# Optimization experiments

Hardware: AMD Instinct MI355X
Metric: run time of the kernel (lower is better)

The kernel has to match this reference:

```python
import jax, jax.numpy as jnp
import numpy as np

EPS = 1e-5
GROUPS = 8


def setup_inputs() -> dict:
    key = jax.random.key(0)
    ks = jax.random.split(key, 7)
    B, C, L = 16, 512, 4096
    x = jax.random.normal(ks[0], (B, C, L), dtype=jnp.float32)
    gamma = jnp.ones((C,), jnp.float32)
    beta = jnp.zeros((C,), jnp.float32)
    # Conv1d kernel_size=1 weights -> plain matrices
    w1 = jax.random.normal(ks[1], (2 * C, C), jnp.float32) / np.sqrt(C)
    b1 = jax.random.normal(ks[2], (2 * C,), jnp.float32) * 0.01
    w2 = jax.random.normal(ks[3], (C, 2 * C), jnp.float32) / np.sqrt(2 * C)
    b2 = jax.random.normal(ks[4], (C,), jnp.float32) * 0.01
    return {"x": x, "gamma": gamma, "beta": beta, "w1": w1, "b1": b1, "w2": w2, "b2": b2}


def _group_norm(x, gamma, beta):
    B, C, L = x.shape
    xg = x.reshape(B, GROUPS, C // GROUPS, L)
    mean = jnp.mean(xg, axis=(2, 3), keepdims=True)
    var = jnp.var(xg, axis=(2, 3), keepdims=True)
    xn = ((xg - mean) * jax.lax.rsqrt(var + EPS)).reshape(B, C, L)
    return xn * gamma[None, :, None] + beta[None, :, None]


def reference(x, gamma, beta, w1, b1, w2, b2):
    h = _group_norm(x, gamma, beta)                      # [B, C, L]
    h = jnp.einsum('bcl,dc->bdl', h, w1) + b1[None, :, None]  # [B, 2C, L]
    h = jax.nn.gelu(h, approximate=False)
    h = jnp.einsum('bdl,cd->bcl', h, w2) + b2[None, :, None]  # [B, C, L]
    return x + h
```

## Files before the change

### kernel.cpp

```cpp
#include <hip/hip_runtime.h>
#include <cstdint>
#include <cstddef>


typedef unsigned short u16;
typedef unsigned int u32;
typedef __attribute__((ext_vector_type(8))) __bf16 bf16x8;
typedef __attribute__((ext_vector_type(4))) float floatx4;

#define BM 128
#define BN 128
#define BKK 64

__device__ __forceinline__ u16 f2bf(float f) {
    union { float f; u32 u; } v; v.f = f;
    u32 u = v.u;
    return (u16)((u + 0x7fffu + ((u >> 16) & 1u)) >> 16);
}

__device__ __forceinline__ float gelu_exact(float v) {
    const float x = fabsf(v) * 0.70710678118654752f;
    const float t = __builtin_amdgcn_rcpf(fmaf(0.3275911f, x, 1.0f));
    float p = fmaf(1.061405429f, t, -1.453152027f);
    p = fmaf(p, t, 1.421413741f);
    p = fmaf(p, t, -0.284496736f);
    p = fmaf(p, t, 0.254829592f);
    p = p * t;
    const float e = __expf(-x * x);
    const float er = fmaf(-p, e, 1.0f);
    const float s = copysignf(er, v);
    return 0.5f * v * (1.0f + s);
}

__device__ __forceinline__ void async_cp16(u16* lds, const u16* g) {
    __builtin_amdgcn_global_load_lds(
        (const __attribute__((address_space(1))) u32*)g,
        (__attribute__((address_space(3))) u32*)lds,
        16, 0, 0);
}

__global__ __launch_bounds__(256) void gn_stats_partial(const float* __restrict__ x,
                                                        float* __restrict__ pstats) {
    const int bx = blockIdx.x;
    const float4* p = (const float4*)(x + (size_t)(bx >> 3) * 262144 + (size_t)(bx & 7) * 32768);
    float s = 0.f, ss = 0.f;
    for (int i = threadIdx.x; i < 8192; i += 256) {
        float4 v = p[i];
        s += v.x + v.y + v.z + v.w;
        ss += v.x * v.x + v.y * v.y + v.z * v.z + v.w * v.w;
    }
#pragma unroll
    for (int off = 32; off > 0; off >>= 1) {
        s  += __shfl_down(s, off, 64);
        ss += __shfl_down(ss, off, 64);
    }
    __shared__ float rs[8];
    const int wv = threadIdx.x >> 6;
    if ((threadIdx.x & 63) == 0) { rs[wv * 2] = s; rs[wv * 2 + 1] = ss; }
    __syncthreads();
    if (threadIdx.x == 0) {
        pstats[bx * 2]     = rs[0] + rs[2] + rs[4] + rs[6];
        pstats[bx * 2 + 1] = rs[1] + rs[3] + rs[5] + rs[7];
    }
}

__global__ __launch_bounds__(256) void conv_w(const float* __restrict__ w1,
                                              const float* __restrict__ w2,
                                              u16* __restrict__ wb) {
    const int idx = (blockIdx.x * 256 + threadIdx.x) * 4;
    const float4 v = (idx < 524288) ? *(const float4*)(w1 + idx)
                                    : *(const float4*)(w2 + (idx - 524288));
    ushort4 o;
    o.x = f2bf(v.x); o.y = f2bf(v.y); o.z = f2bf(v.z); o.w = f2bf(v.w);
    *(ushort4*)(wb + idx) = o;
}

__global__ __launch_bounds__(256) void gn_norm_tr(const float* __restrict__ x,
                                                  const float* __restrict__ gamma,
                                                  const float* __restrict__ beta,
                                                  const float* __restrict__ pstats,
                                                  u16* __restrict__ xnT, int b0) {
    __shared__ u16 T[4][64][72];
    const int bx = blockIdx.x;
    const int l4 = bx & 15;
    const int ct = (bx >> 4) & 7;
    const int bl = bx >> 7;
    const int b = b0 + bl;
    const int c0 = ct * 64, l0 = l4 * 256;
    const int g = ct;
    float S = 0.f, SS = 0.f;
#pragma unroll
    for (int s2 = 0; s2 < 8; ++s2) {
        S  += pstats[((b * 8 + g) * 8 + s2) * 2];
        SS += pstats[((b * 8 + g) * 8 + s2) * 2 + 1];
    }
    const float inv = 1.f / 262144.f;
    const float mean = S * inv;
    const float var = SS * inv - mean * mean;
    const float rstd = rsqrtf(var + 1e-5f);

    const int t = threadIdx.x;
    const int cl = t >> 3;
    const int lo = (t & 7) * 8;
    const int sw = t & 7;
#pragma unroll
    for (int h = 0; h < 2; ++h) {
        const int c = c0 + cl + h * 32;
        const float sc = rstd * gamma[c];
        const float sh = beta[c] - mean * sc;
        const int ccol = cl + h * 32;
        const int col = (((ccol >> 3) ^ sw) << 3) + (ccol & 7);
        const float* srcr = x + ((size_t)(b * 512 + c) * 4096 + l0 + lo);
#pragma unroll
        for (int q = 0; q < 4; ++q) {
            const float* src = srcr + q * 64;
            float4 a = *(const float4*)src;
            float4 bq = *(const float4*)(src + 4);
            float vv[8] = {a.x, a.y, a.z, a.w, bq.x, bq.y, bq.z, bq.w};
#pragma unroll
            for (int k = 0; k < 8; ++k)
                T[q][lo + k][col] = f2bf(fmaf(vv[k], sc, sh));
        }
    }
    __syncthreads();
    const int ll = t >> 3;
    const int co = (t & 7) * 8, cog = t & 7;
#pragma unroll
    for (int h = 0; h < 2; ++h) {
        const int l = ll + h * 32;
        const int colb = (cog ^ ((l >> 3) & 7)) << 3;
#pragma unroll
        for (int q = 0; q < 4; ++q) {
            const uint4* srcv = (const uint4*)&T[q][l][colb];
            *(uint4*)(xnT + ((size_t)(bl * 4096 + l0 + q * 64 + l) * 512 + c0 + co)) = *srcv;
        }
    }
}

__device__ __forceinline__ void gemm_core(const u16* __restrict__ Ag,
                                          const u16* __restrict__ Bg,
                                          int K, floatx4 acc[4][4],
                                          u16* lA, u16* lB,
                                          int wm, int wn, int fr, int quad) {
    const int t = threadIdx.x;

    auto stage = [&](int buf, int kt) {
        u16* dA = lA + buf * (BM * BKK);
        u16* dB = lB + buf * (BN * BKK);
#pragma unroll
        for (int s = 0; s < 4; ++s) {
            int idx = s * 256 + t;
            int row = idx >> 3;
            int kg = (idx & 7) ^ (row & 7);
            async_cp16(dA + idx * 8, Ag + (size_t)row * K + kt + kg * 8);
        }
#pragma unroll
        for (int s = 0; s < 4; ++s) {
            int idx = s * 256 + t;
            int row = idx >> 3;
            int kg = (idx & 7) ^ (row & 7);
            async_cp16(dB + idx * 8, Bg + (size_t)row * K + kt + kg * 8);
        }
    };

    stage(0, 0);
    __syncthreads();
    int cur = 0;
    for (int kt = 0; kt < K; kt += BKK) {
        if (kt + BKK < K) stage(cur ^ 1, kt + BKK);
        const u16* bA = lA + cur * (BM * BKK);
        const u16* bB = lB + cur * (BN * BKK);
#pragma unroll
        for (int kk = 0; kk < BKK; kk += 32) {
            bf16x8 af[4], bb[4];
#pragma unroll
            for (int i = 0; i < 4; ++i) {
                int row = wm + i * 16 + fr;
                int kg = ((kk >> 3) + quad) ^ (fr & 7);
                af[i] = *(const bf16x8*)(bA + row * BKK + kg * 8);
            }
#pragma unroll
            for (int j = 0; j < 4; ++j) {
                int row = wn + j * 16 + fr;
                int kg = ((kk >> 3) + quad) ^ (fr & 7);
                bb[j] = *(const bf16x8*)(bB + row * BKK + kg * 8);
            }
#pragma unroll
            for (int i = 0; i < 4; ++i)
#pragma unroll
                for (int j = 0; j < 4; ++j)
                    acc[i][j] = __builtin_amdgcn_mfma_f32_16x16x32_bf16(bb[j], af[i], acc[i][j], 0, 0, 0);
        }
        __syncthreads();
        cur ^= 1;
    }
}

__global__ __launch_bounds__(256) void gemm1(const u16* __restrict__ xnT,
                                             const u16* __restrict__ w1b,
                                             const float* __restrict__ b1,
                                             u16* __restrict__ h1T) {
    __shared__ uint4 lAq[2 * BM * BKK / 8], lBq[2 * BN * BKK / 8];
    u16* lA = (u16*)lAq; u16* lB = (u16*)lBq;
    const int bx = blockIdx.x;
    const int nt = (bx >> 3) & 7;
    const int mt = (bx & 7) | ((bx >> 6) << 3);
    const int t = threadIdx.x, lane = t & 63, wv = t >> 6;
    const int wm = (wv & 1) * 64, wn = (wv >> 1) * 64;
    const int fr = lane & 15, quad = lane >> 4;
    floatx4 acc[4][4];
#pragma unroll
    for (int i = 0; i < 4; ++i)
#pragma unroll
        for (int j = 0; j < 4; ++j) acc[i][j] = (floatx4){0.f, 0.f, 0.f, 0.f};

    gemm_core(xnT + (size_t)(mt * BM) * 512, w1b + (size_t)(nt * BN) * 512, 512,
              acc, lA, lB, wm, wn, fr, quad);

    const int mb = mt * BM + wm + fr;
    const int nb = nt * BN + wn + quad * 4;
#pragma unroll
    for (int j = 0; j < 4; ++j) {
        const int n0 = nb + j * 16;
        const float4 bv = *(const float4*)(b1 + n0);
#pragma unroll
        for (int i = 0; i < 4; ++i) {
            const int m = mb + i * 16;
            ushort4 o;
            o.x = f2bf(gelu_exact(acc[i][j][0] + bv.x));
            o.y = f2bf(gelu_exact(acc[i][j][1] + bv.y));
            o.z = f2bf(gelu_exact(acc[i][j][2] + bv.z));
            o.w = f2bf(gelu_exact(acc[i][j][3] + bv.w));
            *(ushort4*)(h1T + (size_t)m * 1024 + n0) = o;
        }
    }
}

__global__ __launch_bounds__(256) void gemm2(const u16* __restrict__ w2b,
                                             const u16* __restrict__ h1T,
                                             const float* __restrict__ b2,
                                             const float* __restrict__ x,
                                             float* __restrict__ out, int b0) {
    __shared__ uint4 lAq[2 * BM * BKK / 8], lBq[2 * BN * BKK / 8];
    u16* lA = (u16*)lAq; u16* lB = (u16*)lBq;
    const int bx = blockIdx.x;
    const int mt = (bx >> 3) & 3;
    const int nt = (bx & 7) | ((bx >> 5) << 3);
    const int t = threadIdx.x, lane = t & 63, wv = t >> 6;
    const int wm = (wv & 1) * 64, wn = (wv >> 1) * 64;
    const int fr = lane & 15, quad = lane >> 4;
    floatx4 acc[4][4];
#pragma unroll
    for (int i = 0; i < 4; ++i)
#pragma unroll
        for (int j = 0; j < 4; ++j) acc[i][j] = (floatx4){0.f, 0.f, 0.f, 0.f};

    gemm_core(w2b + (size_t)(mt * BM) * 1024, h1T + (size_t)(nt * BN) * 1024, 1024,
              acc, lA, lB, wm, wn, fr, quad);

    const int n0g = b0 * 4096 + nt * BN;
    const int b = n0g >> 12;
    const int l_base = n0g & 4095;
    const int mb = mt * BM + wm + fr;
    const int nb = wn + quad * 4;
#pragma unroll
    for (int i = 0; i < 4; ++i) {
        const int m = mb + i * 16;
        const float bv = b2[m];
        const size_t rowoff = ((size_t)(b * 512 + m)) * 4096 + l_base + nb;
#pragma unroll
        for (int j = 0; j < 4; ++j) {
            const float4 xv = *(const float4*)(x + rowoff + j * 16);
            float4 ov;
            ov.x = acc[i][j][0] + bv + xv.x;
            ov.y = acc[i][j][1] + bv + xv.y;
            ov.z = acc[i][j][2] + bv + xv.z;
            ov.w = acc[i][j][3] + bv + xv.w;
            *(float4*)(out + rowoff + j * 16) = ov;
        }
    }
}

extern "C" void kernel_launch(void* const* d_in, const int* in_sizes, int n_in,
                              void* d_out, int out_size, void* d_ws, size_t ws_size,
                              hipStream_t stream) {
    const float* x     = (const float*)d_in[0];
    const float* gamma = (const float*)d_in[1];
    const float* beta  = (const float*)d_in[2];
    const float* w1    = (const float*)d_in[3];
    const float* b1    = (const float*)d_in[4];
    const float* w2    = (const float*)d_in[5];
    const float* b2    = (const float*)d_in[6];
    float* out = (float*)d_out;

    char* ws = (char*)d_ws;
    float* pstats = (float*)ws;
    u16* wb = (u16*)(ws + 65536);
    char* chunkbase = ws + 65536 + (2u << 20);
    const size_t fixed = 65536 + (2u << 20);

    const size_t per = (size_t)192 * 1024 * 1024;
    int NC = 16;
    if      (ws_size >= fixed + per)      NC = 1;
    else if (ws_size >= fixed + per / 2)  NC = 2;
    else if (ws_size >= fixed + per / 4)  NC = 4;
    else if (ws_size >= fixed + per / 8)  NC = 8;
    const int CB = 16 / NC;
    u16* xnT = (u16*)chunkbase;
    u16* h1T = (u16*)(chunkbase + (size_t)CB * 4096 * 512 * 2);

    gn_stats_partial<<<1024, 256, 0, stream>>>(x, pstats);
    conv_w<<<1024, 256, 0, stream>>>(w1, w2, wb);
    for (int ch = 0; ch < NC; ++ch) {
        const int b0 = ch * CB;
        gn_norm_tr<<<CB * 128, 256, 0, stream>>>(x, gamma, beta, pstats, xnT, b0);
        gemm1<<<CB * 32 * 8, 256, 0, stream>>>(xnT, wb, b1, h1T);
        gemm2<<<CB * 32 * 4, 256, 0, stream>>>(wb + 524288, h1T, b2, x, out, b0);
    }
}
```

Baseline: 481.8 us.

## Halve GEMM K-tile to 32, merge stats and weight-convert kernels, reorder epilogue

The GEMM K tile drops from 64 to 32, with the LDS swizzle switched to a 4-slot XOR and one MFMA k-step per tile. The aim is to halve LDS use per block, raising occupancy and latency hiding. The cost is twice as many barriers and stage loads per K loop. Separately, the group-norm stats kernel and the weight bf16 conversion are merged into one launch, and the gemm1 epilogue now hoists the bias loads and writes row by row.

New measurement: 513.7 us. 1.07x slower.

```diff
diff --git a/kernel.cpp b/kernel.cpp
--- a/kernel.cpp
+++ b/kernel.cpp
@@ -10,7 +10,7 @@
 
 #define BM 128
 #define BN 128
-#define BKK 64
+#define BKK 32
 
 __device__ __forceinline__ u16 f2bf(float f) {
     union { float f; u32 u; } v; v.f = f;
@@ -39,9 +39,21 @@
         16, 0, 0);
 }
 
-__global__ __launch_bounds__(256) void gn_stats_partial(const float* __restrict__ x,
-                                                        float* __restrict__ pstats) {
+__global__ __launch_bounds__(256) void gn_stats_w(const float* __restrict__ x,
+                                                  float* __restrict__ pstats,
+                                                  const float* __restrict__ w1,
+                                                  const float* __restrict__ w2,
+                                                  u16* __restrict__ wb) {
     const int bx = blockIdx.x;
+    if (bx >= 1024) {
+        const int idx = ((bx - 1024) * 256 + threadIdx.x) * 4;
+        const float4 v = (idx < 524288) ? *(const float4*)(w1 + idx)
+                                        : *(const float4*)(w2 + (idx - 524288));
+        ushort4 o;
+        o.x = f2bf(v.x); o.y = f2bf(v.y); o.z = f2bf(v.z); o.w = f2bf(v.w);
+        *(ushort4*)(wb + idx) = o;
+        return;
+    }
     const float4* p = (const float4*)(x + (size_t)(bx >> 3) * 262144 + (size_t)(bx & 7) * 32768);
     float s = 0.f, ss = 0.f;
     for (int i = threadIdx.x; i < 8192; i += 256) {
@@ -62,17 +74,6 @@
         pstats[bx * 2]     = rs[0] + rs[2] + rs[4] + rs[6];
         pstats[bx * 2 + 1] = rs[1] + rs[3] + rs[5] + rs[7];
     }
-}
-
-__global__ __launch_bounds__(256) void conv_w(const float* __restrict__ w1,
-                                              const float* __restrict__ w2,
-                                              u16* __restrict__ wb) {
-    const int idx = (blockIdx.x * 256 + threadIdx.x) * 4;
-    const float4 v = (idx < 524288) ? *(const float4*)(w1 + idx)
-                                    : *(const float4*)(w2 + (idx - 524288));
-    ushort4 o;
-    o.x = f2bf(v.x); o.y = f2bf(v.y); o.z = f2bf(v.z); o.w = f2bf(v.w);
-    *(ushort4*)(wb + idx) = o;
 }
 
 __global__ __launch_bounds__(256) void gn_norm_tr(const float* __restrict__ x,
@@ -148,17 +149,17 @@
         u16* dA = lA + buf * (BM * BKK);
         u16* dB = lB + buf * (BN * BKK);
 #pragma unroll
-        for (int s = 0; s < 4; ++s) {
+        for (int s = 0; s < 2; ++s) {
             int idx = s * 256 + t;
-            int row = idx >> 3;
-            int kg = (idx & 7) ^ (row & 7);
+            int row = idx >> 2;
+            int kg = (idx & 3) ^ (row & 3);
             async_cp16(dA + idx * 8, Ag + (size_t)row * K + kt + kg * 8);
         }
 #pragma unroll
-        for (int s = 0; s < 4; ++s) {
+        for (int s = 0; s < 2; ++s) {
             int idx = s * 256 + t;
-            int row = idx >> 3;
-            int kg = (idx & 7) ^ (row & 7);
+            int row = idx >> 2;
+            int kg = (idx & 3) ^ (row & 3);
             async_cp16(dB + idx * 8, Bg + (size_t)row * K + kt + kg * 8);
         }
     };
@@ -166,31 +167,29 @@
     stage(0, 0);
     __syncthreads();
     int cur = 0;
+    const int sl = quad;
     for (int kt = 0; kt < K; kt += BKK) {
         if (kt + BKK < K) stage(cur ^ 1, kt + BKK);
         const u16* bA = lA + cur * (BM * BKK);
         const u16* bB = lB + cur * (BN * BKK);
-#pragma unroll
-        for (int kk = 0; kk < BKK; kk += 32) {
-            bf16x8 af[4], bb[4];
-#pragma unroll
-            for (int i = 0; i < 4; ++i) {
-                int row = wm + i * 16 + fr;
-                int kg = ((kk >> 3) + quad) ^ (fr & 7);
-                af[i] = *(const bf16x8*)(bA + row * BKK + kg * 8);
-            }
-#pragma unroll
-            for (int j = 0; j < 4; ++j) {
-                int row = wn + j * 16 + fr;
-                int kg = ((kk >> 3) + quad) ^ (fr & 7);
-                bb[j] = *(const bf16x8*)(bB + row * BKK + kg * 8);
-            }
-#pragma unroll
-            for (int i = 0; i < 4; ++i)
-#pragma unroll
-                for (int j = 0; j < 4; ++j)
-                    acc[i][j] = __builtin_amdgcn_mfma_f32_16x16x32_bf16(bb[j], af[i], acc[i][j], 0, 0, 0);
-        }
+        bf16x8 af[4], bb[4];
+#pragma unroll
+        for (int i = 0; i < 4; ++i) {
+            int row = wm + i * 16 + fr;
+            int slot = sl ^ (fr & 3);
+            af[i] = *(const bf16x8*)(bA + row * BKK + slot * 8);
+        }
+#pragma unroll
+        for (int j = 0; j < 4; ++j) {
+            int row = wn + j * 16 + fr;
+            int slot = sl ^ (fr & 3);
+            bb[j] = *(const bf16x8*)(bB + row * BKK + slot * 8);
+        }
+#pragma unroll
+        for (int i = 0; i < 4; ++i)
+#pragma unroll
+            for (int j = 0; j < 4; ++j)
+                acc[i][j] = __builtin_amdgcn_mfma_f32_16x16x32_bf16(bb[j], af[i], acc[i][j], 0, 0, 0);
         __syncthreads();
         cur ^= 1;
     }
@@ -219,19 +218,21 @@
 
     const int mb = mt * BM + wm + fr;
     const int nb = nt * BN + wn + quad * 4;
-#pragma unroll
-    for (int j = 0; j < 4; ++j) {
-        const int n0 = nb + j * 16;
-        const float4 bv = *(const float4*)(b1 + n0);
-#pragma unroll
-        for (int i = 0; i < 4; ++i) {
-            const int m = mb + i * 16;
+    float4 bv[4];
+#pragma unroll
+    for (int j = 0; j < 4; ++j) bv[j] = *(const float4*)(b1 + nb + j * 16);
+#pragma unroll
+    for (int i = 0; i < 4; ++i) {
+        const int m = mb + i * 16;
+        u16* drow = h1T + (size_t)m * 1024 + nb;
+#pragma unroll
+        for (int j = 0; j < 4; ++j) {
             ushort4 o;
-            o.x = f2bf(gelu_exact(acc[i][j][0] + bv.x));
-            o.y = f2bf(gelu_exact(acc[i][j][1] + bv.y));
-            o.z = f2bf(gelu_exact(acc[i][j][2] + bv.z));
-            o.w = f2bf(gelu_exact(acc[i][j][3] + bv.w));
-            *(ushort4*)(h1T + (size_t)m * 1024 + n0) = o;
+            o.x = f2bf(gelu_exact(acc[i][j][0] + bv[j].x));
+            o.y = f2bf(gelu_exact(acc[i][j][1] + bv[j].y));
+            o.z = f2bf(gelu_exact(acc[i][j][2] + bv[j].z));
+            o.w = f2bf(gelu_exact(acc[i][j][3] + bv[j].w));
+            *(ushort4*)(drow + j * 16) = o;
         }
     }
 }
@@ -309,8 +310,7 @@
     u16* xnT = (u16*)chunkbase;
     u16* h1T = (u16*)(chunkbase + (size_t)CB * 4096 * 512 * 2);
 
-    gn_stats_partial<<<1024, 256, 0, stream>>>(x, pstats);
-    conv_w<<<1024, 256, 0, stream>>>(w1, w2, wb);
+    gn_stats_w<<<2048, 256, 0, stream>>>(x, pstats, w1, w2, wb);
     for (int ch = 0; ch < NC; ++ch) {
         const int b0 = ch * CB;
         gn_norm_tr<<<CB * 128, 256, 0, stream>>>(x, gamma, beta, pstats, xnT, b0);
```
